# Optimization experiments

Measured on AMD Instinct MI355X. Metric: run time of the kernel, lower is better.

Reference implementation:

```python
import jax, jax.numpy as jnp
import numpy as np

B, P, ED, AD, DD, E, V, T = 64, 196, 2048, 512, 512, 300, 1000, 96


def setup_inputs() -> dict:
    key = jax.random.key(0)
    ks = jax.random.split(key, 24)
    s = 0.02  # small init scale for weights
    lens = jax.random.randint(ks[2], (B,), 2, T + 1).astype(jnp.int32)
    lens = lens.at[0].set(T)  # ensure max(decode_lengths) == T-1 (static)
    return {
        'encoder_out': jax.random.normal(ks[0], (B, P, ED), jnp.float32),
        'encoded_captions': jax.random.randint(ks[1], (B, T), 0, V),
        'caption_lengths': lens,
        'emb': jax.random.uniform(ks[3], (V, E), jnp.float32, -0.1, 0.1),
        'W_enc_att': jax.random.normal(ks[4], (ED, AD), jnp.float32) * s,
        'b_enc_att': jnp.zeros((AD,), jnp.float32),
        'W_dec_att': jax.random.normal(ks[5], (DD, AD), jnp.float32) * s,
        'b_dec_att': jnp.zeros((AD,), jnp.float32),
        'w_full': jax.random.normal(ks[6], (AD,), jnp.float32) * s,
        'b_full': jnp.zeros((), jnp.float32),
        'W_init_h': jax.random.normal(ks[7], (ED, DD), jnp.float32) * s,
        'b_init_h': jnp.zeros((DD,), jnp.float32),
        'W_init_c': jax.random.normal(ks[8], (ED, DD), jnp.float32) * s,
        'b_init_c': jnp.zeros((DD,), jnp.float32),
        'W_fbeta': jax.random.normal(ks[9], (DD, ED), jnp.float32) * s,
        'b_fbeta': jnp.zeros((ED,), jnp.float32),
        'W_ih': jax.random.normal(ks[10], (E + ED, 4 * DD), jnp.float32) * s,
        'b_ih': jnp.zeros((4 * DD,), jnp.float32),
        'W_hh': jax.random.normal(ks[11], (DD, 4 * DD), jnp.float32) * s,
        'b_hh': jnp.zeros((4 * DD,), jnp.float32),
        'W_fc': jax.random.uniform(ks[12], (DD, V), jnp.float32, -0.1, 0.1),
        'b_fc': jnp.zeros((V,), jnp.float32),
    }


def reference(encoder_out, encoded_captions, caption_lengths, emb,
              W_enc_att, b_enc_att, W_dec_att, b_dec_att, w_full, b_full,
              W_init_h, b_init_h, W_init_c, b_init_c, W_fbeta, b_fbeta,
              W_ih, b_ih, W_hh, b_hh, W_fc, b_fc):
    # Sort by caption length, descending (stable like torch.sort on ints)
    sort_ind = jnp.argsort(-caption_lengths)
    lens = caption_lengths[sort_ind]
    eo = encoder_out[sort_ind]                  # [B,P,ED]
    caps = encoded_captions[sort_ind]           # [B,T]
    decode_lengths = lens - 1                   # [B]

    embs = emb[caps]                            # [B,T,E]
    mean_eo = eo.mean(axis=1)                   # [B,ED]
    h0 = mean_eo @ W_init_h + b_init_h          # [B,DD]
    c0 = mean_eo @ W_init_c + b_init_c

    # encoder-side attention projection is step-invariant: hoist it
    att1 = eo @ W_enc_att + b_enc_att           # [B,P,AD]

    Tdec = T - 1
    ts = jnp.arange(Tdec)
    masks = (decode_lengths[None, :] > ts[:, None]).astype(eo.dtype)  # [Tdec,B]
    emb_seq = jnp.swapaxes(embs[:, :Tdec, :], 0, 1)                    # [Tdec,B,E]

    def step(carry, xs):
        h, c = carry
        emb_t, m = xs                           # [B,E], [B]
        mb = m[:, None]
        # Bahdanau attention
        att2 = h @ W_dec_att + b_dec_att        # [B,AD]
        e = jnp.einsum('bpa,a->bp', jax.nn.relu(att1 + att2[:, None, :]), w_full) + b_full
        alpha = jax.nn.softmax(e, axis=1)       # [B,P]
        awe = jnp.einsum('bpd,bp->bd', eo, alpha)  # [B,ED]
        gate = jax.nn.sigmoid(h @ W_fbeta + b_fbeta)
        x = jnp.concatenate([emb_t, gate * awe], axis=1)  # [B,E+ED]
        # LSTMCell (torch gate order: i, f, g, o)
        gates = x @ W_ih + b_ih + h @ W_hh + b_hh
        i, f, g, o = jnp.split(gates, 4, axis=1)
        c_new = jax.nn.sigmoid(f) * c + jax.nn.sigmoid(i) * jnp.tanh(g)
        h_new = jax.nn.sigmoid(o) * jnp.tanh(c_new)
        # only active rows (sorted so they are a prefix) update state
        h2 = mb * h_new + (1.0 - mb) * h
        c2 = mb * c_new + (1.0 - mb) * c
        preds = (h2 @ W_fc + b_fc) * mb         # dropout = identity (eval)
        return (h2, c2), (preds, alpha * mb)

    (_, _), (preds, alphas) = jax.lax.scan(step, (h0, c0), (emb_seq, masks))
    predictions = jnp.swapaxes(preds, 0, 1)     # [B,Tdec,V]
    alphas = jnp.swapaxes(alphas, 0, 1)         # [B,Tdec,P]
    return predictions, caps, decode_lengths, alphas, sort_ind
```

## Files before the change

kernel.cpp:

```cpp
#include <hip/hip_runtime.h>
#include <stddef.h>
#include <math.h>

static constexpr int B = 64, P = 196, ED = 2048, AD = 512, DD = 512, E = 300, V = 1000, T = 96, TD = 95;
static constexpr int KX = E + ED;
static constexpr int KTOT = KX + DD;
static constexpr int KSPLIT = 8;
static constexpr int KPER = 368;
static constexpr int NG = 4 * DD;

static constexpr size_t POFF   = 0;
static constexpr size_t CAPOFF = (size_t)B * TD * V;
static constexpr size_t DLOFF  = CAPOFF + (size_t)B * T;
static constexpr size_t AOFF   = DLOFF + B;
static constexpr size_t SOFF   = AOFF + (size_t)B * TD * P;

__device__ __forceinline__ float sigm(float x) { return 1.0f / (1.0f + expf(-x)); }

__global__ __launch_bounds__(64) void k_sort(const int* __restrict__ lens,
                                             const int* __restrict__ caps_in,
                                             int* __restrict__ sidx,
                                             int* __restrict__ dlen,
                                             int* __restrict__ caps_s,
                                             float* __restrict__ out) {
    __shared__ int sl[B];
    __shared__ int ss[B];
    int i = threadIdx.x;
    sl[i] = lens[i];
    __syncthreads();
    int li = sl[i];
    int r = 0;
    for (int j = 0; j < B; j++) {
        int lj = sl[j];
        r += (lj > li) || (lj == li && j < i);
    }
    ss[r] = i;
    sidx[r] = i;
    dlen[r] = li - 1;
    out[DLOFF + r] = (float)(li - 1);
    out[SOFF + r] = (float)i;
    __syncthreads();
    for (int idx = i; idx < B * T; idx += B) {
        int b = idx / T, tt = idx % T;
        int v = caps_in[ss[b] * T + tt];
        caps_s[idx] = v;
        out[CAPOFF + idx] = (float)v;
    }
}

__global__ __launch_bounds__(256) void k_mean(const float* __restrict__ eo,
                                              const int* __restrict__ sidx,
                                              float* __restrict__ mean_eo) {
    int b = blockIdx.y;
    int d = blockIdx.x * 256 + threadIdx.x;
    const float* base = eo + ((size_t)sidx[b] * P) * ED + d;
    float s = 0.f;
    for (int p = 0; p < P; p++) s += base[(size_t)p * ED];
    mean_eo[(size_t)b * ED + d] = s * (1.0f / (float)P);
}

__global__ __launch_bounds__(256) void k_init(const float* __restrict__ mean_eo,
                                              const float* __restrict__ Wh, const float* __restrict__ bh,
                                              const float* __restrict__ Wc, const float* __restrict__ bc,
                                              float* __restrict__ h0, float* __restrict__ c0,
                                              float* __restrict__ xT) {
    int idx = blockIdx.x * 256 + threadIdx.x;
    int b = idx >> 9, j = idx & 511;
    const float* m = mean_eo + (size_t)b * ED;
    float ah = bh[j], ac = bc[j];
    for (int k = 0; k < ED; k++) {
        float mv = m[k];
        ah += mv * Wh[(size_t)k * DD + j];
        ac += mv * Wc[(size_t)k * DD + j];
    }
    h0[idx] = ah;
    c0[idx] = ac;
    xT[(size_t)(KX + j) * B + b] = ah;
}

__global__ __launch_bounds__(256) void k_att1(const float* __restrict__ eo,
                                              const float* __restrict__ W,
                                              const float* __restrict__ bias,
                                              const int* __restrict__ sidx,
                                              float* __restrict__ att1) {
    int m0 = blockIdx.x * 64, n0 = blockIdx.y * 64;
    __shared__ float sA[16][68];
    __shared__ float sB[16][68];
    int tid = threadIdx.x;
    int tx = tid & 15, ty = tid >> 4;
    float acc[4][4] = {};

    int la_m = tid >> 2;
    int la_k = (tid & 3) * 4;
    int lb_k = tid >> 4;
    int lb_n = (tid & 15) * 4;

    int mA = m0 + la_m;
    int bA = mA / P, pA = mA % P;
    const float* arow = eo + ((size_t)sidx[bA] * P + pA) * ED;

    for (int k0 = 0; k0 < ED; k0 += 16) {
        float4 av = *(const float4*)(arow + k0 + la_k);
        sA[la_k + 0][la_m] = av.x;
        sA[la_k + 1][la_m] = av.y;
        sA[la_k + 2][la_m] = av.z;
        sA[la_k + 3][la_m] = av.w;
        float4 bv = *(const float4*)(W + (size_t)(k0 + lb_k) * AD + n0 + lb_n);
        *(float4*)&sB[lb_k][lb_n] = bv;
        __syncthreads();
#pragma unroll
        for (int kk = 0; kk < 16; kk++) {
            float4 a4 = *(const float4*)&sA[kk][ty * 4];
            float4 b4 = *(const float4*)&sB[kk][tx * 4];
            float av_[4] = {a4.x, a4.y, a4.z, a4.w};
            float bv_[4] = {b4.x, b4.y, b4.z, b4.w};
#pragma unroll
            for (int i = 0; i < 4; i++)
#pragma unroll
                for (int j = 0; j < 4; j++) acc[i][j] += av_[i] * bv_[j];
        }
        __syncthreads();
    }
#pragma unroll
    for (int i = 0; i < 4; i++) {
        int m = m0 + ty * 4 + i;
        int n = n0 + tx * 4;
        float4 o;
        o.x = acc[i][0] + bias[n + 0];
        o.y = acc[i][1] + bias[n + 1];
        o.z = acc[i][2] + bias[n + 2];
        o.w = acc[i][3] + bias[n + 3];
        *(float4*)(att1 + (size_t)m * AD + n) = o;
    }
}

__global__ __launch_bounds__(256) void kA1(const float* __restrict__ hprev,
                                           const float* __restrict__ Wda, const float* __restrict__ bda,
                                           const float* __restrict__ Wfb, const float* __restrict__ bfb,
                                           const float* __restrict__ emb,
                                           const int* __restrict__ caps_s,
                                           float* __restrict__ att2g,
                                           float* __restrict__ fg,
                                           float* __restrict__ xT, int t) {
    int bx = blockIdx.x;
    int tid = threadIdx.x;
    if (bx >= 80) {
        int k0 = (bx - 80) * 60;
        for (int l = tid; l < 60 * 64; l += 256) {
            int r = l >> 6, b = l & 63;
            int k = k0 + r;
            int cap = caps_s[b * T + t];
            xT[(size_t)k * B + b] = emb[(size_t)cap * E + k];
        }
        return;
    }
    int n0 = bx * 32;
    bool is_att = (n0 < AD);
    __shared__ float sH[16][68];
    __shared__ float sW[16][36];
    float acc[4][2] = {};
    int tb = tid & 15, tn = tid >> 4;

    for (int k0 = 0; k0 < DD; k0 += 16) {
        {
            int b = tid >> 2, q = tid & 3;
            float4 hv = *(const float4*)(hprev + (size_t)b * DD + k0 + q * 4);
            sH[q * 4 + 0][b] = hv.x;
            sH[q * 4 + 1][b] = hv.y;
            sH[q * 4 + 2][b] = hv.z;
            sH[q * 4 + 3][b] = hv.w;
        }
        if (tid < 128) {
            int kk = tid >> 3, nn = (tid & 7) * 4;
            float4 wv;
            if (is_att) wv = *(const float4*)(Wda + (size_t)(k0 + kk) * AD + n0 + nn);
            else        wv = *(const float4*)(Wfb + (size_t)(k0 + kk) * ED + (n0 - AD) + nn);
            *(float4*)&sW[kk][nn] = wv;
        }
        __syncthreads();
#pragma unroll
        for (int kk = 0; kk < 16; kk++) {
            float4 hv = *(const float4*)&sH[kk][tb * 4];
            float w0 = sW[kk][tn * 2 + 0];
            float w1 = sW[kk][tn * 2 + 1];
            acc[0][0] += hv.x * w0; acc[0][1] += hv.x * w1;
            acc[1][0] += hv.y * w0; acc[1][1] += hv.y * w1;
            acc[2][0] += hv.z * w0; acc[2][1] += hv.z * w1;
            acc[3][0] += hv.w * w0; acc[3][1] += hv.w * w1;
        }
        __syncthreads();
    }
#pragma unroll
    for (int i = 0; i < 4; i++)
#pragma unroll
        for (int j = 0; j < 2; j++) {
            int b = tb * 4 + i;
            int n = n0 + tn * 2 + j;
            float v = acc[i][j];
            if (is_att) att2g[(size_t)b * AD + n] = v + bda[n];
            else {
                int d = n - AD;
                fg[(size_t)b * ED + d] = sigm(v + bfb[d]);
            }
        }
}

__global__ __launch_bounds__(256) void kA2(const float* __restrict__ att2g,
                                           const float* __restrict__ att1,
                                           const float* __restrict__ wf,
                                           const float* __restrict__ bfv,
                                           const int* __restrict__ dlen,
                                           float* __restrict__ alpha,
                                           float* __restrict__ out, int t) {
    int b = blockIdx.x;
    int tid = threadIdx.x;
    __shared__ float sa2[AD];
    __shared__ float swf[AD];
    __shared__ float se[P];
    __shared__ float red[256];

    sa2[tid] = att2g[(size_t)b * AD + tid];
    sa2[tid + 256] = att2g[(size_t)b * AD + tid + 256];
    swf[tid] = wf[tid];
    swf[tid + 256] = wf[tid + 256];
    __syncthreads();

    int w = tid >> 6, lane = tid & 63;
    float bf0 = bfv[0];
    for (int p = w; p < P; p += 4) {
        const float* row = att1 + ((size_t)b * P + p) * AD + lane * 8;
        float4 u0 = *(const float4*)row;
        float4 u1 = *(const float4*)(row + 4);
        float4 s0 = *(const float4*)&sa2[lane * 8];
        float4 s1 = *(const float4*)&sa2[lane * 8 + 4];
        float4 w0 = *(const float4*)&swf[lane * 8];
        float4 w1 = *(const float4*)&swf[lane * 8 + 4];
        float acc = fmaxf(u0.x + s0.x, 0.f) * w0.x + fmaxf(u0.y + s0.y, 0.f) * w0.y +
                    fmaxf(u0.z + s0.z, 0.f) * w0.z + fmaxf(u0.w + s0.w, 0.f) * w0.w +
                    fmaxf(u1.x + s1.x, 0.f) * w1.x + fmaxf(u1.y + s1.y, 0.f) * w1.y +
                    fmaxf(u1.z + s1.z, 0.f) * w1.z + fmaxf(u1.w + s1.w, 0.f) * w1.w;
#pragma unroll
        for (int m = 32; m >= 1; m >>= 1) acc += __shfl_xor(acc, m, 64);
        if (lane == 0) se[p] = acc + bf0;
    }
    __syncthreads();

    red[tid] = (tid < P) ? se[tid] : -1e30f;
    __syncthreads();
    for (int s = 128; s > 0; s >>= 1) {
        if (tid < s) red[tid] = fmaxf(red[tid], red[tid + s]);
        __syncthreads();
    }
    float mx = red[0];
    __syncthreads();
    float ex = (tid < P) ? expf(se[tid] - mx) : 0.f;
    red[tid] = ex;
    __syncthreads();
    for (int s = 128; s > 0; s >>= 1) {
        if (tid < s) red[tid] += red[tid + s];
        __syncthreads();
    }
    float inv = 1.0f / red[0];
    if (tid < P) {
        float a = ex * inv;
        alpha[(size_t)b * P + tid] = a;
        float m = (dlen[b] > t) ? 1.f : 0.f;
        out[AOFF + ((size_t)b * TD + t) * P + tid] = a * m;
    }
}

__global__ __launch_bounds__(256) void kB(const float* __restrict__ eo,
                                          const int* __restrict__ sidx,
                                          const float* __restrict__ alpha,
                                          const float* __restrict__ fg,
                                          float* __restrict__ xT) {
    int b = blockIdx.y, ch = blockIdx.x, tid = threadIdx.x;
    __shared__ float sal[P];
    if (tid < P) sal[tid] = alpha[(size_t)b * P + tid];
    __syncthreads();
    int d = ch * 256 + tid;
    const float* base = eo + ((size_t)sidx[b] * P) * ED + d;
    float aw = 0.f;
    for (int p = 0; p < P; p++) aw += base[(size_t)p * ED] * sal[p];
    xT[(size_t)(E + d) * B + b] = fg[(size_t)b * ED + d] * aw;
}

__global__ __launch_bounds__(256) void kC(const float* __restrict__ xT,
                                          const float* __restrict__ Wih,
                                          const float* __restrict__ Whh,
                                          float* __restrict__ part) {
    int bx = blockIdx.x;
    int ks = bx >> 6, nb = bx & 63;
    int n0 = nb * 32;
    int tid = threadIdx.x;
    int tb = tid & 15, tn = tid >> 4;
    __shared__ float sW[16][36];
    float acc[4][2] = {};
    int kbase = ks * KPER;

    for (int tile = 0; tile < 23; tile++) {
        int k0 = kbase + tile * 16;
        if (tid < 128) {
            int kk = tid >> 3, nn = (tid & 7) * 4;
            int kg = k0 + kk;
            float4 wv = make_float4(0.f, 0.f, 0.f, 0.f);
            if (kg < KX) wv = *(const float4*)&Wih[(size_t)kg * NG + n0 + nn];
            else if (kg < KTOT) wv = *(const float4*)&Whh[(size_t)(kg - KX) * NG + n0 + nn];
            *(float4*)&sW[kk][nn] = wv;
        }
        __syncthreads();
#pragma unroll
        for (int kk = 0; kk < 16; kk++) {
            int kg = k0 + kk;
            float4 xv = make_float4(0.f, 0.f, 0.f, 0.f);
            if (kg < KTOT) xv = *(const float4*)&xT[(size_t)kg * B + tb * 4];
            float w0 = sW[kk][tn * 2 + 0];
            float w1 = sW[kk][tn * 2 + 1];
            acc[0][0] += xv.x * w0; acc[0][1] += xv.x * w1;
            acc[1][0] += xv.y * w0; acc[1][1] += xv.y * w1;
            acc[2][0] += xv.z * w0; acc[2][1] += xv.z * w1;
            acc[3][0] += xv.w * w0; acc[3][1] += xv.w * w1;
        }
        __syncthreads();
    }
    float* pr = part + (size_t)ks * B * NG;
#pragma unroll
    for (int i = 0; i < 4; i++)
#pragma unroll
        for (int j = 0; j < 2; j++) {
            int b = tb * 4 + i, n = n0 + tn * 2 + j;
            pr[(size_t)b * NG + n] = acc[i][j];
        }
}

__global__ __launch_bounds__(256) void kD(const float* __restrict__ part,
                                          const float* __restrict__ bih,
                                          const float* __restrict__ bhh,
                                          const float* __restrict__ hprev,
                                          const float* __restrict__ cc,
                                          const int* __restrict__ dlen,
                                          float* __restrict__ hseq_t,
                                          float* __restrict__ cn,
                                          float* __restrict__ xT, int t) {
    int idx = blockIdx.x * 256 + threadIdx.x;
    int b = idx >> 9, j = idx & 511;
    float gi = bih[j] + bhh[j];
    float gf = bih[DD + j] + bhh[DD + j];
    float gg = bih[2 * DD + j] + bhh[2 * DD + j];
    float go = bih[3 * DD + j] + bhh[3 * DD + j];
#pragma unroll
    for (int s = 0; s < KSPLIT; s++) {
        const float* pr = part + ((size_t)s * B + b) * NG;
        gi += pr[j];
        gf += pr[DD + j];
        gg += pr[2 * DD + j];
        go += pr[3 * DD + j];
    }
    float cold = cc[idx], hold = hprev[idx];
    float cnew = sigm(gf) * cold + sigm(gi) * tanhf(gg);
    float hnew = sigm(go) * tanhf(cnew);
    bool m = dlen[b] > t;
    float h2 = m ? hnew : hold;
    float c2 = m ? cnew : cold;
    hseq_t[idx] = h2;
    cn[idx] = c2;
    xT[(size_t)(KX + j) * B + b] = h2;
}

__global__ __launch_bounds__(256) void k_predsall(const float* __restrict__ hseq,
                                                  const float* __restrict__ Wfc,
                                                  const float* __restrict__ bfc,
                                                  const int* __restrict__ dlen,
                                                  float* __restrict__ out) {
    int t = blockIdx.x;
    int n0 = blockIdx.y * 64;
    int tid = threadIdx.x;
    int tx = tid & 15, ty = tid >> 4;
    __shared__ float sA[16][68];
    __shared__ float sB[16][68];
    float acc[4][4] = {};
    const float* A = hseq + (size_t)t * B * DD;

    for (int k0 = 0; k0 < DD; k0 += 16) {
        {
            int b = tid >> 2, q = tid & 3;
            float4 hv = *(const float4*)(A + (size_t)b * DD + k0 + q * 4);
            sA[q * 4 + 0][b] = hv.x;
            sA[q * 4 + 1][b] = hv.y;
            sA[q * 4 + 2][b] = hv.z;
            sA[q * 4 + 3][b] = hv.w;
        }
        {
            int kk = tid >> 4, nn = (tid & 15) * 4;
            int c = n0 + nn;
            const float* wrow = Wfc + (size_t)(k0 + kk) * V;
            float4 wv;
            if (c + 3 < V) wv = *(const float4*)(wrow + c);
            else {
                wv.x = (c + 0 < V) ? wrow[c + 0] : 0.f;
                wv.y = (c + 1 < V) ? wrow[c + 1] : 0.f;
                wv.z = (c + 2 < V) ? wrow[c + 2] : 0.f;
                wv.w = (c + 3 < V) ? wrow[c + 3] : 0.f;
            }
            *(float4*)&sB[kk][nn] = wv;
        }
        __syncthreads();
#pragma unroll
        for (int kk = 0; kk < 16; kk++) {
            float4 a4 = *(const float4*)&sA[kk][ty * 4];
            float4 b4 = *(const float4*)&sB[kk][tx * 4];
            float av_[4] = {a4.x, a4.y, a4.z, a4.w};
            float bv_[4] = {b4.x, b4.y, b4.z, b4.w};
#pragma unroll
            for (int i = 0; i < 4; i++)
#pragma unroll
                for (int j = 0; j < 4; j++) acc[i][j] += av_[i] * bv_[j];
        }
        __syncthreads();
    }
#pragma unroll
    for (int i = 0; i < 4; i++) {
        int b = ty * 4 + i;
        bool m = dlen[b] > t;
#pragma unroll
        for (int j = 0; j < 4; j++) {
            int n = n0 + tx * 4 + j;
            if (n < V)
                out[POFF + ((size_t)b * TD + t) * V + n] = m ? (acc[i][j] + bfc[n]) : 0.f;
        }
    }
}

extern "C" void kernel_launch(void* const* d_in, const int* in_sizes, int n_in,
                              void* d_out, int out_size, void* d_ws, size_t ws_size,
                              hipStream_t stream) {
    const float* eo    = (const float*)d_in[0];
    const int*   caps  = (const int*)d_in[1];
    const int*   lens  = (const int*)d_in[2];
    const float* emb   = (const float*)d_in[3];
    const float* Wea   = (const float*)d_in[4];
    const float* bea   = (const float*)d_in[5];
    const float* Wda   = (const float*)d_in[6];
    const float* bda   = (const float*)d_in[7];
    const float* wfull = (const float*)d_in[8];
    const float* bfull = (const float*)d_in[9];
    const float* Wih_  = (const float*)d_in[10];
    const float* bih_  = (const float*)d_in[11];
    const float* Wic   = (const float*)d_in[12];
    const float* bic   = (const float*)d_in[13];
    const float* Wfb   = (const float*)d_in[14];
    const float* bfb   = (const float*)d_in[15];
    const float* Wih   = (const float*)d_in[16];
    const float* bih   = (const float*)d_in[17];
    const float* Whh   = (const float*)d_in[18];
    const float* bhh   = (const float*)d_in[19];
    const float* Wfc   = (const float*)d_in[20];
    const float* bfc   = (const float*)d_in[21];
    float* out = (float*)d_out;

    char* w = (char*)d_ws;
    auto carve = [&](size_t bytes) -> void* {
        void* p = (void*)w;
        w += (bytes + 255) & ~(size_t)255;
        return p;
    };
    int* sidx      = (int*)carve(B * 4);
    int* dlen      = (int*)carve(B * 4);
    int* caps_s    = (int*)carve((size_t)B * T * 4);
    float* mean_eo = (float*)carve((size_t)B * ED * 4);
    float* h0      = (float*)carve((size_t)B * DD * 4);
    float* cb0     = (float*)carve((size_t)B * DD * 4);
    float* cb1     = (float*)carve((size_t)B * DD * 4);
    float* att1    = (float*)carve((size_t)B * P * AD * 4);
    float* alphaW  = (float*)carve((size_t)B * P * 4);
    float* att2g   = (float*)carve((size_t)B * AD * 4);
    float* fg      = (float*)carve((size_t)B * ED * 4);
    float* xT      = (float*)carve((size_t)KTOT * B * 4);
    float* part    = (float*)carve((size_t)KSPLIT * B * NG * 4);
    float* hseq    = (float*)carve((size_t)TD * B * DD * 4);
    float* cb[2] = {cb0, cb1};

    k_sort<<<1, 64, 0, stream>>>(lens, caps, sidx, dlen, caps_s, out);
    k_mean<<<dim3(ED / 256, B), 256, 0, stream>>>(eo, sidx, mean_eo);
    k_init<<<(B * DD) / 256, 256, 0, stream>>>(mean_eo, Wih_, bih_, Wic, bic, h0, cb0, xT);
    k_att1<<<dim3((B * P) / 64, AD / 64), 256, 0, stream>>>(eo, Wea, bea, sidx, att1);

    for (int t = 0; t < TD; t++) {
        const float* hprev = (t == 0) ? h0 : (hseq + (size_t)(t - 1) * B * DD);
        float* cc = cb[t & 1];
        float* cn = cb[(t + 1) & 1];
        kA1<<<85, 256, 0, stream>>>(hprev, Wda, bda, Wfb, bfb, emb, caps_s, att2g, fg, xT, t);
        kA2<<<64, 256, 0, stream>>>(att2g, att1, wfull, bfull, dlen, alphaW, out, t);
        kB<<<dim3(8, B), 256, 0, stream>>>(eo, sidx, alphaW, fg, xT);
        kC<<<512, 256, 0, stream>>>(xT, Wih, Whh, part);
        kD<<<(B * DD) / 256, 256, 0, stream>>>(part, bih, bhh, hprev, cc, dlen,
                                               hseq + (size_t)t * B * DD, cn, xT, t);
    }
    k_predsall<<<dim3(TD, 16), 256, 0, stream>>>(hseq, Wfc, bfc, dlen, out);
}
```

Baseline: 19.47 ms.

## Fuse per-step decoder kernels into one persistent kernel with grid barriers

Replaces the five kernel launches per decode step with a single persistent kernel of 256 blocks that runs every timestep and separates the phases with a software grid barrier built on atomics. It also pre-converts the sorted encoder output to bf16 when workspace allows, which halves the memory traffic of the per-step attention-weighted sum. The LSTM input is switched to row-major and the gate GEMM is retiled to 4x4 register tiles. This removes launch overhead across 95 steps. In exchange it adds spin-wait barrier costs, depends on all 256 blocks being co-resident to avoid deadlock, and loses precision in the awe computation.

```diff
diff --git a/kernel.cpp b/kernel.cpp
--- a/kernel.cpp
+++ b/kernel.cpp
@@ -1,4 +1,5 @@
 #include <hip/hip_runtime.h>
+#include <hip/hip_bf16.h>
 #include <stddef.h>
 #include <math.h>
 
@@ -8,6 +9,7 @@
 static constexpr int KSPLIT = 8;
 static constexpr int KPER = 368;
 static constexpr int NG = 4 * DD;
+static constexpr int NBLK = 256;
 
 static constexpr size_t POFF   = 0;
 static constexpr size_t CAPOFF = (size_t)B * TD * V;
@@ -16,6 +18,24 @@
 static constexpr size_t SOFF   = AOFF + (size_t)B * TD * P;
 
 __device__ __forceinline__ float sigm(float x) { return 1.0f / (1.0f + expf(-x)); }
+
+__device__ __forceinline__ void gbar(int* cnt, int* gen) {
+    __syncthreads();
+    if (threadIdx.x == 0) {
+        __threadfence();
+        int g = __hip_atomic_load(gen, __ATOMIC_RELAXED, __HIP_MEMORY_SCOPE_AGENT);
+        int a = __hip_atomic_fetch_add(cnt, 1, __ATOMIC_ACQ_REL, __HIP_MEMORY_SCOPE_AGENT);
+        if (a == NBLK - 1) {
+            __hip_atomic_store(cnt, 0, __ATOMIC_RELAXED, __HIP_MEMORY_SCOPE_AGENT);
+            __hip_atomic_store(gen, g + 1, __ATOMIC_RELEASE, __HIP_MEMORY_SCOPE_AGENT);
+        } else {
+            while (__hip_atomic_load(gen, __ATOMIC_ACQUIRE, __HIP_MEMORY_SCOPE_AGENT) <= g)
+                __builtin_amdgcn_s_sleep(2);
+        }
+        __threadfence();
+    }
+    __syncthreads();
+}
 
 __global__ __launch_bounds__(64) void k_sort(const int* __restrict__ lens,
                                              const int* __restrict__ caps_in,
@@ -63,7 +83,7 @@
                                               const float* __restrict__ Wh, const float* __restrict__ bh,
                                               const float* __restrict__ Wc, const float* __restrict__ bc,
                                               float* __restrict__ h0, float* __restrict__ c0,
-                                              float* __restrict__ xT) {
+                                              float* __restrict__ xR) {
     int idx = blockIdx.x * 256 + threadIdx.x;
     int b = idx >> 9, j = idx & 511;
     const float* m = mean_eo + (size_t)b * ED;
@@ -75,7 +95,7 @@
     }
     h0[idx] = ah;
     c0[idx] = ac;
-    xT[(size_t)(KX + j) * B + b] = ah;
+    xR[(size_t)b * KTOT + KX + j] = ah;
 }
 
 __global__ __launch_bounds__(256) void k_att1(const float* __restrict__ eo,
@@ -134,237 +154,268 @@
     }
 }
 
-__global__ __launch_bounds__(256) void kA1(const float* __restrict__ hprev,
-                                           const float* __restrict__ Wda, const float* __restrict__ bda,
-                                           const float* __restrict__ Wfb, const float* __restrict__ bfb,
-                                           const float* __restrict__ emb,
-                                           const int* __restrict__ caps_s,
-                                           float* __restrict__ att2g,
-                                           float* __restrict__ fg,
-                                           float* __restrict__ xT, int t) {
-    int bx = blockIdx.x;
-    int tid = threadIdx.x;
-    if (bx >= 80) {
-        int k0 = (bx - 80) * 60;
-        for (int l = tid; l < 60 * 64; l += 256) {
-            int r = l >> 6, b = l & 63;
-            int k = k0 + r;
-            int cap = caps_s[b * T + t];
-            xT[(size_t)k * B + b] = emb[(size_t)cap * E + k];
-        }
-        return;
-    }
-    int n0 = bx * 32;
-    bool is_att = (n0 < AD);
-    __shared__ float sH[16][68];
-    __shared__ float sW[16][36];
-    float acc[4][2] = {};
-    int tb = tid & 15, tn = tid >> 4;
-
-    for (int k0 = 0; k0 < DD; k0 += 16) {
+__global__ __launch_bounds__(256) void k_eob(const float* __restrict__ eo,
+                                             const int* __restrict__ sidx,
+                                             __hip_bfloat16* __restrict__ eob) {
+    int row = blockIdx.x;
+    int b = row / P, p = row - b * P;
+    const float* src = eo + ((size_t)sidx[b] * P + p) * ED;
+    __hip_bfloat16* dst = eob + (size_t)row * ED;
+    for (int d = threadIdx.x; d < ED; d += 256) dst[d] = __float2bfloat16(src[d]);
+}
+
+__global__ __launch_bounds__(256, 1) void k_loop(
+    const float* __restrict__ eo, const __hip_bfloat16* __restrict__ eob,
+    const int* __restrict__ sidx, const int* __restrict__ dlen,
+    const int* __restrict__ caps_s, const float* __restrict__ emb,
+    const float* __restrict__ Wda, const float* __restrict__ bda,
+    const float* __restrict__ Wfb, const float* __restrict__ bfb,
+    const float* __restrict__ wfull, const float* __restrict__ bfull,
+    const float* __restrict__ Wih, const float* __restrict__ Whh,
+    const float* __restrict__ bih, const float* __restrict__ bhh,
+    const float* __restrict__ att1, const float* __restrict__ h0,
+    float* __restrict__ hseq, float* __restrict__ cb0, float* __restrict__ cb1,
+    float* __restrict__ att2g, float* __restrict__ fg, float* __restrict__ alpha,
+    float* __restrict__ xR, float* __restrict__ part,
+    float* __restrict__ out, int* __restrict__ bar) {
+    __shared__ float smem[2176];
+    int bid = blockIdx.x, tid = threadIdx.x;
+    int* cnt = bar;
+    int* gen = bar + 16;
+
+    for (int t = 0; t < TD; t++) {
+        const float* hprev = (t == 0) ? h0 : (hseq + (size_t)(t - 1) * B * DD);
+        float* cc = (t & 1) ? cb1 : cb0;
+        float* cn = (t & 1) ? cb0 : cb1;
+
+        if (bid < 160) {
+            bool is_att = (bid < 32);
+            int n0 = is_att ? bid * 16 : (bid - 32) * 16;
+            float* sH = smem;
+            float* sW = smem + 1088;
+            int tb = tid & 15, tn = tid >> 4;
+            float acc[4] = {0.f, 0.f, 0.f, 0.f};
+            int sb = tid >> 2, sq = tid & 3;
+            int wk = tid >> 4, wn = tid & 15;
+            for (int k0 = 0; k0 < DD; k0 += 16) {
+                float4 hv = *(const float4*)(hprev + (size_t)sb * DD + k0 + sq * 4);
+                sH[(sq * 4 + 0) * 68 + sb] = hv.x;
+                sH[(sq * 4 + 1) * 68 + sb] = hv.y;
+                sH[(sq * 4 + 2) * 68 + sb] = hv.z;
+                sH[(sq * 4 + 3) * 68 + sb] = hv.w;
+                float wv;
+                if (is_att) wv = Wda[(size_t)(k0 + wk) * AD + n0 + wn];
+                else        wv = Wfb[(size_t)(k0 + wk) * ED + n0 + wn];
+                sW[wk * 17 + wn] = wv;
+                __syncthreads();
+#pragma unroll
+                for (int kk = 0; kk < 16; kk++) {
+                    float4 h4 = *(const float4*)&sH[kk * 68 + tb * 4];
+                    float w = sW[kk * 17 + tn];
+                    acc[0] += h4.x * w;
+                    acc[1] += h4.y * w;
+                    acc[2] += h4.z * w;
+                    acc[3] += h4.w * w;
+                }
+                __syncthreads();
+            }
+            int n = n0 + tn;
+            if (is_att) {
+                float bv = bda[n];
+#pragma unroll
+                for (int i = 0; i < 4; i++)
+                    att2g[(size_t)(tb * 4 + i) * AD + n] = acc[i] + bv;
+            } else {
+                float bv = bfb[n];
+#pragma unroll
+                for (int i = 0; i < 4; i++)
+                    fg[(size_t)(tb * 4 + i) * ED + n] = sigm(acc[i] + bv);
+            }
+        } else if (bid < 165) {
+            int k0 = (bid - 160) * 60;
+            int r = tid & 63, bq = tid >> 6;
+            if (r < 60) {
+                for (int pass = 0; pass < 16; pass++) {
+                    int b = pass * 4 + bq;
+                    int cap = caps_s[b * T + t];
+                    xR[(size_t)b * KTOT + k0 + r] = emb[(size_t)cap * E + k0 + r];
+                }
+            }
+        }
+        gbar(cnt, gen);
+
+        if (bid < B) {
+            int b = bid;
+            float* sa2 = smem;
+            float* swf = smem + 512;
+            float* se = smem + 1024;
+            float* red = smem + 1232;
+            sa2[tid] = att2g[(size_t)b * AD + tid];
+            sa2[tid + 256] = att2g[(size_t)b * AD + tid + 256];
+            swf[tid] = wfull[tid];
+            swf[tid + 256] = wfull[tid + 256];
+            __syncthreads();
+            int wv = tid >> 6, lane = tid & 63;
+            float bf0 = bfull[0];
+            for (int p = wv; p < P; p += 4) {
+                const float* row = att1 + ((size_t)b * P + p) * AD + lane * 8;
+                float4 u0 = *(const float4*)row;
+                float4 u1 = *(const float4*)(row + 4);
+                float4 s0 = *(const float4*)&sa2[lane * 8];
+                float4 s1 = *(const float4*)&sa2[lane * 8 + 4];
+                float4 w0 = *(const float4*)&swf[lane * 8];
+                float4 w1 = *(const float4*)&swf[lane * 8 + 4];
+                float acc = fmaxf(u0.x + s0.x, 0.f) * w0.x + fmaxf(u0.y + s0.y, 0.f) * w0.y +
+                            fmaxf(u0.z + s0.z, 0.f) * w0.z + fmaxf(u0.w + s0.w, 0.f) * w0.w +
+                            fmaxf(u1.x + s1.x, 0.f) * w1.x + fmaxf(u1.y + s1.y, 0.f) * w1.y +
+                            fmaxf(u1.z + s1.z, 0.f) * w1.z + fmaxf(u1.w + s1.w, 0.f) * w1.w;
+#pragma unroll
+                for (int m = 32; m >= 1; m >>= 1) acc += __shfl_xor(acc, m, 64);
+                if (lane == 0) se[p] = acc + bf0;
+            }
+            __syncthreads();
+            red[tid] = (tid < P) ? se[tid] : -1e30f;
+            __syncthreads();
+            for (int s = 128; s > 0; s >>= 1) {
+                if (tid < s) red[tid] = fmaxf(red[tid], red[tid + s]);
+                __syncthreads();
+            }
+            float mx = red[0];
+            __syncthreads();
+            float ex = (tid < P) ? expf(se[tid] - mx) : 0.f;
+            red[tid] = ex;
+            __syncthreads();
+            for (int s = 128; s > 0; s >>= 1) {
+                if (tid < s) red[tid] += red[tid + s];
+                __syncthreads();
+            }
+            float inv = 1.0f / red[0];
+            if (tid < P) {
+                float a = ex * inv;
+                alpha[(size_t)b * P + tid] = a;
+                float m = (dlen[b] > t) ? 1.f : 0.f;
+                out[AOFF + ((size_t)b * TD + t) * P + tid] = a * m;
+            }
+        }
+        gbar(cnt, gen);
+
         {
-            int b = tid >> 2, q = tid & 3;
-            float4 hv = *(const float4*)(hprev + (size_t)b * DD + k0 + q * 4);
-            sH[q * 4 + 0][b] = hv.x;
-            sH[q * 4 + 1][b] = hv.y;
-            sH[q * 4 + 2][b] = hv.z;
-            sH[q * 4 + 3][b] = hv.w;
-        }
+            int b = bid >> 2, dq = bid & 3;
+            float* sal = smem;
+            if (tid < P) sal[tid] = alpha[(size_t)b * P + tid];
+            __syncthreads();
+            int d = dq * 512 + tid * 2;
+            float a0 = 0.f, a1 = 0.f;
+            if (eob) {
+                const __hip_bfloat16* base = eob + ((size_t)b * P) * ED + d;
+                for (int p = 0; p < P; p++) {
+                    __hip_bfloat162 v = *(const __hip_bfloat162*)(base + (size_t)p * ED);
+                    float2 f = __bfloat1622float2(v);
+                    float al = sal[p];
+                    a0 += f.x * al;
+                    a1 += f.y * al;
+                }
+            } else {
+                const float* base = eo + ((size_t)sidx[b] * P) * ED + d;
+                for (int p = 0; p < P; p++) {
+                    float2 f = *(const float2*)(base + (size_t)p * ED);
+                    float al = sal[p];
+                    a0 += f.x * al;
+                    a1 += f.y * al;
+                }
+            }
+            float2 g2 = *(const float2*)&fg[(size_t)b * ED + d];
+            float2 o;
+            o.x = a0 * g2.x;
+            o.y = a1 * g2.y;
+            *(float2*)&xR[(size_t)b * KTOT + E + d] = o;
+        }
+        gbar(cnt, gen);
+
+        {
+            int ks = bid >> 5, nt = bid & 31;
+            int n0 = nt * 64;
+            float* sX = smem;
+            float* sW = smem + 1088;
+            int tb = tid & 15, tn = tid >> 4;
+            float acc[4][4] = {};
+            int kbase = ks * KPER;
+            int sb = tid >> 2, sq = tid & 3;
+            int wk = tid >> 4, wn4 = (tid & 15) * 4;
+            for (int tile = 0; tile < 23; tile++) {
+                int k0 = kbase + tile * 16;
+                {
+                    int kg = k0 + sq * 4;
+                    float4 xv;
+                    if (kg + 3 < KTOT) xv = *(const float4*)(xR + (size_t)sb * KTOT + kg);
+                    else {
+                        xv.x = (kg + 0 < KTOT) ? xR[(size_t)sb * KTOT + kg + 0] : 0.f;
+                        xv.y = (kg + 1 < KTOT) ? xR[(size_t)sb * KTOT + kg + 1] : 0.f;
+                        xv.z = (kg + 2 < KTOT) ? xR[(size_t)sb * KTOT + kg + 2] : 0.f;
+                        xv.w = (kg + 3 < KTOT) ? xR[(size_t)sb * KTOT + kg + 3] : 0.f;
+                    }
+                    sX[(sq * 4 + 0) * 68 + sb] = xv.x;
+                    sX[(sq * 4 + 1) * 68 + sb] = xv.y;
+                    sX[(sq * 4 + 2) * 68 + sb] = xv.z;
+                    sX[(sq * 4 + 3) * 68 + sb] = xv.w;
+                }
+                {
+                    int kg = k0 + wk;
+                    float4 wv = make_float4(0.f, 0.f, 0.f, 0.f);
+                    if (kg < KX) wv = *(const float4*)(Wih + (size_t)kg * NG + n0 + wn4);
+                    else if (kg < KTOT) wv = *(const float4*)(Whh + (size_t)(kg - KX) * NG + n0 + wn4);
+                    *(float4*)&sW[wk * 68 + wn4] = wv;
+                }
+                __syncthreads();
+#pragma unroll
+                for (int kk = 0; kk < 16; kk++) {
+                    float4 xv = *(const float4*)&sX[kk * 68 + tb * 4];
+                    float4 wv = *(const float4*)&sW[kk * 68 + tn * 4];
+                    float xa[4] = {xv.x, xv.y, xv.z, xv.w};
+                    float wa[4] = {wv.x, wv.y, wv.z, wv.w};
+#pragma unroll
+                    for (int i = 0; i < 4; i++)
+#pragma unroll
+                        for (int j = 0; j < 4; j++) acc[i][j] += xa[i] * wa[j];
+                }
+                __syncthreads();
+            }
+            float* pr = part + (size_t)ks * B * NG;
+#pragma unroll
+            for (int i = 0; i < 4; i++) {
+                float4 o = make_float4(acc[i][0], acc[i][1], acc[i][2], acc[i][3]);
+                *(float4*)&pr[(size_t)(tb * 4 + i) * NG + n0 + tn * 4] = o;
+            }
+        }
+        gbar(cnt, gen);
+
         if (tid < 128) {
-            int kk = tid >> 3, nn = (tid & 7) * 4;
-            float4 wv;
-            if (is_att) wv = *(const float4*)(Wda + (size_t)(k0 + kk) * AD + n0 + nn);
-            else        wv = *(const float4*)(Wfb + (size_t)(k0 + kk) * ED + (n0 - AD) + nn);
-            *(float4*)&sW[kk][nn] = wv;
-        }
-        __syncthreads();
-#pragma unroll
-        for (int kk = 0; kk < 16; kk++) {
-            float4 hv = *(const float4*)&sH[kk][tb * 4];
-            float w0 = sW[kk][tn * 2 + 0];
-            float w1 = sW[kk][tn * 2 + 1];
-            acc[0][0] += hv.x * w0; acc[0][1] += hv.x * w1;
-            acc[1][0] += hv.y * w0; acc[1][1] += hv.y * w1;
-            acc[2][0] += hv.z * w0; acc[2][1] += hv.z * w1;
-            acc[3][0] += hv.w * w0; acc[3][1] += hv.w * w1;
-        }
-        __syncthreads();
-    }
-#pragma unroll
-    for (int i = 0; i < 4; i++)
-#pragma unroll
-        for (int j = 0; j < 2; j++) {
-            int b = tb * 4 + i;
-            int n = n0 + tn * 2 + j;
-            float v = acc[i][j];
-            if (is_att) att2g[(size_t)b * AD + n] = v + bda[n];
-            else {
-                int d = n - AD;
-                fg[(size_t)b * ED + d] = sigm(v + bfb[d]);
-            }
-        }
-}
-
-__global__ __launch_bounds__(256) void kA2(const float* __restrict__ att2g,
-                                           const float* __restrict__ att1,
-                                           const float* __restrict__ wf,
-                                           const float* __restrict__ bfv,
-                                           const int* __restrict__ dlen,
-                                           float* __restrict__ alpha,
-                                           float* __restrict__ out, int t) {
-    int b = blockIdx.x;
-    int tid = threadIdx.x;
-    __shared__ float sa2[AD];
-    __shared__ float swf[AD];
-    __shared__ float se[P];
-    __shared__ float red[256];
-
-    sa2[tid] = att2g[(size_t)b * AD + tid];
-    sa2[tid + 256] = att2g[(size_t)b * AD + tid + 256];
-    swf[tid] = wf[tid];
-    swf[tid + 256] = wf[tid + 256];
-    __syncthreads();
-
-    int w = tid >> 6, lane = tid & 63;
-    float bf0 = bfv[0];
-    for (int p = w; p < P; p += 4) {
-        const float* row = att1 + ((size_t)b * P + p) * AD + lane * 8;
-        float4 u0 = *(const float4*)row;
-        float4 u1 = *(const float4*)(row + 4);
-        float4 s0 = *(const float4*)&sa2[lane * 8];
-        float4 s1 = *(const float4*)&sa2[lane * 8 + 4];
-        float4 w0 = *(const float4*)&swf[lane * 8];
-        float4 w1 = *(const float4*)&swf[lane * 8 + 4];
-        float acc = fmaxf(u0.x + s0.x, 0.f) * w0.x + fmaxf(u0.y + s0.y, 0.f) * w0.y +
-                    fmaxf(u0.z + s0.z, 0.f) * w0.z + fmaxf(u0.w + s0.w, 0.f) * w0.w +
-                    fmaxf(u1.x + s1.x, 0.f) * w1.x + fmaxf(u1.y + s1.y, 0.f) * w1.y +
-                    fmaxf(u1.z + s1.z, 0.f) * w1.z + fmaxf(u1.w + s1.w, 0.f) * w1.w;
-#pragma unroll
-        for (int m = 32; m >= 1; m >>= 1) acc += __shfl_xor(acc, m, 64);
-        if (lane == 0) se[p] = acc + bf0;
-    }
-    __syncthreads();
-
-    red[tid] = (tid < P) ? se[tid] : -1e30f;
-    __syncthreads();
-    for (int s = 128; s > 0; s >>= 1) {
-        if (tid < s) red[tid] = fmaxf(red[tid], red[tid + s]);
-        __syncthreads();
-    }
-    float mx = red[0];
-    __syncthreads();
-    float ex = (tid < P) ? expf(se[tid] - mx) : 0.f;
-    red[tid] = ex;
-    __syncthreads();
-    for (int s = 128; s > 0; s >>= 1) {
-        if (tid < s) red[tid] += red[tid + s];
-        __syncthreads();
-    }
-    float inv = 1.0f / red[0];
-    if (tid < P) {
-        float a = ex * inv;
-        alpha[(size_t)b * P + tid] = a;
-        float m = (dlen[b] > t) ? 1.f : 0.f;
-        out[AOFF + ((size_t)b * TD + t) * P + tid] = a * m;
-    }
-}
-
-__global__ __launch_bounds__(256) void kB(const float* __restrict__ eo,
-                                          const int* __restrict__ sidx,
-                                          const float* __restrict__ alpha,
-                                          const float* __restrict__ fg,
-                                          float* __restrict__ xT) {
-    int b = blockIdx.y, ch = blockIdx.x, tid = threadIdx.x;
-    __shared__ float sal[P];
-    if (tid < P) sal[tid] = alpha[(size_t)b * P + tid];
-    __syncthreads();
-    int d = ch * 256 + tid;
-    const float* base = eo + ((size_t)sidx[b] * P) * ED + d;
-    float aw = 0.f;
-    for (int p = 0; p < P; p++) aw += base[(size_t)p * ED] * sal[p];
-    xT[(size_t)(E + d) * B + b] = fg[(size_t)b * ED + d] * aw;
-}
-
-__global__ __launch_bounds__(256) void kC(const float* __restrict__ xT,
-                                          const float* __restrict__ Wih,
-                                          const float* __restrict__ Whh,
-                                          float* __restrict__ part) {
-    int bx = blockIdx.x;
-    int ks = bx >> 6, nb = bx & 63;
-    int n0 = nb * 32;
-    int tid = threadIdx.x;
-    int tb = tid & 15, tn = tid >> 4;
-    __shared__ float sW[16][36];
-    float acc[4][2] = {};
-    int kbase = ks * KPER;
-
-    for (int tile = 0; tile < 23; tile++) {
-        int k0 = kbase + tile * 16;
-        if (tid < 128) {
-            int kk = tid >> 3, nn = (tid & 7) * 4;
-            int kg = k0 + kk;
-            float4 wv = make_float4(0.f, 0.f, 0.f, 0.f);
-            if (kg < KX) wv = *(const float4*)&Wih[(size_t)kg * NG + n0 + nn];
-            else if (kg < KTOT) wv = *(const float4*)&Whh[(size_t)(kg - KX) * NG + n0 + nn];
-            *(float4*)&sW[kk][nn] = wv;
-        }
-        __syncthreads();
-#pragma unroll
-        for (int kk = 0; kk < 16; kk++) {
-            int kg = k0 + kk;
-            float4 xv = make_float4(0.f, 0.f, 0.f, 0.f);
-            if (kg < KTOT) xv = *(const float4*)&xT[(size_t)kg * B + tb * 4];
-            float w0 = sW[kk][tn * 2 + 0];
-            float w1 = sW[kk][tn * 2 + 1];
-            acc[0][0] += xv.x * w0; acc[0][1] += xv.x * w1;
-            acc[1][0] += xv.y * w0; acc[1][1] += xv.y * w1;
-            acc[2][0] += xv.z * w0; acc[2][1] += xv.z * w1;
-            acc[3][0] += xv.w * w0; acc[3][1] += xv.w * w1;
-        }
-        __syncthreads();
-    }
-    float* pr = part + (size_t)ks * B * NG;
-#pragma unroll
-    for (int i = 0; i < 4; i++)
-#pragma unroll
-        for (int j = 0; j < 2; j++) {
-            int b = tb * 4 + i, n = n0 + tn * 2 + j;
-            pr[(size_t)b * NG + n] = acc[i][j];
-        }
-}
-
-__global__ __launch_bounds__(256) void kD(const float* __restrict__ part,
-                                          const float* __restrict__ bih,
-                                          const float* __restrict__ bhh,
-                                          const float* __restrict__ hprev,
-                                          const float* __restrict__ cc,
-                                          const int* __restrict__ dlen,
-                                          float* __restrict__ hseq_t,
-                                          float* __restrict__ cn,
-                                          float* __restrict__ xT, int t) {
-    int idx = blockIdx.x * 256 + threadIdx.x;
-    int b = idx >> 9, j = idx & 511;
-    float gi = bih[j] + bhh[j];
-    float gf = bih[DD + j] + bhh[DD + j];
-    float gg = bih[2 * DD + j] + bhh[2 * DD + j];
-    float go = bih[3 * DD + j] + bhh[3 * DD + j];
-#pragma unroll
-    for (int s = 0; s < KSPLIT; s++) {
-        const float* pr = part + ((size_t)s * B + b) * NG;
-        gi += pr[j];
-        gf += pr[DD + j];
-        gg += pr[2 * DD + j];
-        go += pr[3 * DD + j];
-    }
-    float cold = cc[idx], hold = hprev[idx];
-    float cnew = sigm(gf) * cold + sigm(gi) * tanhf(gg);
-    float hnew = sigm(go) * tanhf(cnew);
-    bool m = dlen[b] > t;
-    float h2 = m ? hnew : hold;
-    float c2 = m ? cnew : cold;
-    hseq_t[idx] = h2;
-    cn[idx] = c2;
-    xT[(size_t)(KX + j) * B + b] = h2;
+            int idx = bid * 128 + tid;
+            int b = idx >> 9, j = idx & 511;
+            float gi = bih[j] + bhh[j];
+            float gf = bih[DD + j] + bhh[DD + j];
+            float gg = bih[2 * DD + j] + bhh[2 * DD + j];
+            float go = bih[3 * DD + j] + bhh[3 * DD + j];
+#pragma unroll
+            for (int s = 0; s < KSPLIT; s++) {
+                const float* pr = part + ((size_t)s * B + b) * NG;
+                gi += pr[j];
+                gf += pr[DD + j];
+                gg += pr[2 * DD + j];
+                go += pr[3 * DD + j];
+            }
+            float cold = cc[idx], hold = hprev[idx];
+            float cnew = sigm(gf) * cold + sigm(gi) * tanhf(gg);
+            float hnew = sigm(go) * tanhf(cnew);
+            bool m = dlen[b] > t;
+            float h2 = m ? hnew : hold;
+            float c2 = m ? cnew : cold;
+            hseq[(size_t)t * B * DD + idx] = h2;
+            cn[idx] = c2;
+            xR[(size_t)b * KTOT + KX + j] = h2;
+        }
+        gbar(cnt, gen);
+    }
 }
 
 __global__ __launch_bounds__(256) void k_predsall(const float* __restrict__ hseq,
@@ -458,12 +509,14 @@
     const float* bfc   = (const float*)d_in[21];
     float* out = (float*)d_out;
 
-    char* w = (char*)d_ws;
+    char* w0 = (char*)d_ws;
+    char* w = w0;
     auto carve = [&](size_t bytes) -> void* {
         void* p = (void*)w;
         w += (bytes + 255) & ~(size_t)255;
         return p;
     };
+    int* bar       = (int*)carve(256);
     int* sidx      = (int*)carve(B * 4);
     int* dlen      = (int*)carve(B * 4);
     int* caps_s    = (int*)carve((size_t)B * T * 4);
@@ -475,26 +528,26 @@
     float* alphaW  = (float*)carve((size_t)B * P * 4);
     float* att2g   = (float*)carve((size_t)B * AD * 4);
     float* fg      = (float*)carve((size_t)B * ED * 4);
-    float* xT      = (float*)carve((size_t)KTOT * B * 4);
+    float* xR      = (float*)carve((size_t)B * KTOT * 4);
     float* part    = (float*)carve((size_t)KSPLIT * B * NG * 4);
     float* hseq    = (float*)carve((size_t)TD * B * DD * 4);
-    float* cb[2] = {cb0, cb1};
+    size_t eob_bytes = (size_t)B * P * ED * 2;
+    __hip_bfloat16* eob = nullptr;
+    size_t used = (size_t)(w - w0);
+    if (used + eob_bytes + 256 <= ws_size)
+        eob = (__hip_bfloat16*)carve(eob_bytes);
 
     k_sort<<<1, 64, 0, stream>>>(lens, caps, sidx, dlen, caps_s, out);
     k_mean<<<dim3(ED / 256, B), 256, 0, stream>>>(eo, sidx, mean_eo);
-    k_init<<<(B * DD) / 256, 256, 0, stream>>>(mean_eo, Wih_, bih_, Wic, bic, h0, cb0, xT);
+    k_init<<<(B * DD) / 256, 256, 0, stream>>>(mean_eo, Wih_, bih_, Wic, bic, h0, cb0, xR);
     k_att1<<<dim3((B * P) / 64, AD / 64), 256, 0, stream>>>(eo, Wea, bea, sidx, att1);
-
-    for (int t = 0; t < TD; t++) {
-        const float* hprev = (t == 0) ? h0 : (hseq + (size_t)(t - 1) * B * DD);
-        float* cc = cb[t & 1];
-        float* cn = cb[(t + 1) & 1];
-        kA1<<<85, 256, 0, stream>>>(hprev, Wda, bda, Wfb, bfb, emb, caps_s, att2g, fg, xT, t);
-        kA2<<<64, 256, 0, stream>>>(att2g, att1, wfull, bfull, dlen, alphaW, out, t);
-        kB<<<dim3(8, B), 256, 0, stream>>>(eo, sidx, alphaW, fg, xT);
-        kC<<<512, 256, 0, stream>>>(xT, Wih, Whh, part);
-        kD<<<(B * DD) / 256, 256, 0, stream>>>(part, bih, bhh, hprev, cc, dlen,
-                                               hseq + (size_t)t * B * DD, cn, xT, t);
-    }
+    if (eob) k_eob<<<B * P, 256, 0, stream>>>(eo, sidx, eob);
+
+    hipMemsetAsync(bar, 0, 256, stream);
+    k_loop<<<NBLK, 256, 0, stream>>>(eo, eob, sidx, dlen, caps_s, emb,
+                                     Wda, bda, Wfb, bfb, wfull, bfull,
+                                     Wih, Whh, bih, bhh, att1, h0,
+                                     hseq, cb0, cb1, att2g, fg, alphaW,
+                                     xR, part, out, bar);
     k_predsall<<<dim3(TD, 16), 256, 0, stream>>>(hseq, Wfc, bfc, dlen, out);
 }
```

After: 38.43 ms. 1.97x slower.
